# Kernel optimization log

Measured on AMD Instinct MI355X. Metric: run time of the kernel, lower is better.

## Reference

```python
import jax, jax.numpy as jnp
import numpy as np

EMBED_SIZE = 512
SCALE = EMBED_SIZE ** 0.5  # note: sqrt(embed_size), not sqrt(head_dim), per source


def setup_inputs() -> dict:
    key = jax.random.key(0)
    kq, kk, kv = jax.random.split(key, 3)
    B, H, S, D = 4, 8, 2048, 64
    query = jax.random.normal(kq, (B, H, S, D), dtype=jnp.float32)
    key_t = jax.random.normal(kk, (B, H, S, D), dtype=jnp.float32)
    value = jax.random.normal(kv, (B, S, H, D), dtype=jnp.float32)  # [b, kv_len, h, d]
    return {"query": query, "key": key_t, "value": value}


def reference(query, key, value):
    # scores: [b, h, q, k]
    scores = jnp.einsum('bhqf,bhkf->bhqk', query, key)
    weight = jax.nn.softmax(scores / SCALE, axis=3)
    # value is [b, l, h, d]; output [b, q, h, d]
    out = jnp.einsum('bhql,blhd->bqhd', weight, value)
    return out
```

## Files before the change

### kernel.cpp

```cpp
#include <hip/hip_runtime.h>
#include <stdint.h>

#define NB 4
#define NH 8
#define NS 2048
#define ND 64
#define BQ 128
#define TK 64
#define KP 72
#define NG 2
#define NITG (NS/(TK*NG))
#define SLOT (TK*KP + ND*KP)

typedef __bf16  bf16x8 __attribute__((ext_vector_type(8)));
typedef float   f32x16 __attribute__((ext_vector_type(16)));

__device__ __forceinline__ uint32_t pkbf(float x, float y) {
  uint32_t ax = __builtin_bit_cast(uint32_t, x) + 0x8000u;
  uint32_t ay = __builtin_bit_cast(uint32_t, y) + 0x8000u;
  return __builtin_amdgcn_perm(ay, ax, 0x07060302u);
}
__device__ __forceinline__ unsigned short bfu(float x) {
  return (unsigned short)((__builtin_bit_cast(uint32_t, x) + 0x8000u) >> 16);
}

__global__ __launch_bounds__(256) void prep(
    const float* __restrict__ K, const float* __restrict__ V,
    unsigned short* __restrict__ Kh, unsigned short* __restrict__ Vth)
{
  __shared__ unsigned short T[64*72];
  const int t = threadIdx.x;
  const int blk = blockIdx.x;
  const int bh = blk >> 5, st = blk & 31;
  const int s0 = st*64;
  const int b = bh>>3, hh = bh&7;

  {
    const float* kin = K + ((size_t)bh*NS + s0)*ND + t*16;
    unsigned short* kout = Kh + ((size_t)bh*NS + s0)*ND + t*16;
    float4 a0 = ((const float4*)kin)[0], a1 = ((const float4*)kin)[1];
    float4 a2 = ((const float4*)kin)[2], a3 = ((const float4*)kin)[3];
    uint4 w0 = make_uint4(pkbf(a0.x,a0.y),pkbf(a0.z,a0.w),pkbf(a1.x,a1.y),pkbf(a1.z,a1.w));
    uint4 w1 = make_uint4(pkbf(a2.x,a2.y),pkbf(a2.z,a2.w),pkbf(a3.x,a3.y),pkbf(a3.z,a3.w));
    ((uint4*)kout)[0] = w0; ((uint4*)kout)[1] = w1;
  }

  {
    const int vrow = t>>2, vq = t&3;
    const float* vp = V + (((size_t)b*NS + s0 + vrow)*NH + hh)*ND + 4*vq;
#pragma unroll
    for (int j=0;j<4;++j){
      float4 v = *(const float4*)(vp + 16*j);
      int d0 = 16*j + 4*vq;
      T[(size_t)(d0+0)*72 + vrow] = bfu(v.x);
      T[(size_t)(d0+1)*72 + vrow] = bfu(v.y);
      T[(size_t)(d0+2)*72 + vrow] = bfu(v.z);
      T[(size_t)(d0+3)*72 + vrow] = bfu(v.w);
    }
  }
  __syncthreads();
  {
    const int dd = t>>2, wq = t&3;
    unsigned short* vout = Vth + ((size_t)bh*ND + dd)*NS + s0 + 16*wq;
    uint4 o0 = *(const uint4*)&T[(size_t)dd*72 + 16*wq];
    uint4 o1 = *(const uint4*)&T[(size_t)dd*72 + 16*wq + 8];
    ((uint4*)vout)[0] = o0; ((uint4*)vout)[1] = o1;
  }
}

__global__ __launch_bounds__(512, 4) void fa_fwd(
    const float* __restrict__ Q, const unsigned short* __restrict__ Kh,
    const unsigned short* __restrict__ Vth, float* __restrict__ O)
{
  __shared__ __attribute__((aligned(16))) unsigned short SMEM[NG*2*SLOT];

  const int tid = threadIdx.x, wid = tid>>6, lane = tid&63;
  const int l31 = lane&31, h = lane>>5;
  const int g = wid>>2, qs = wid&3;
  const int t4 = tid & 255;

  const int bid = blockIdx.x;
  const int logical = (bid & 7)*64 + (bid >> 3);
  const int bh = logical >> 4;
  const int q0 = (logical & 15) * BQ;
  const int b = bh>>3, hh = bh&7;

  const float*          Qb  = Q   + ((size_t)bh*NS + q0)*ND;
  const unsigned short* Kb  = Kh  + (size_t)bh*NS*ND;
  const unsigned short* Vtb = Vth + (size_t)bh*ND*NS;
  float*                Ob  = O   + ((size_t)b*NS*NH + hh)*ND;

  const float kSc = 1.44269504088896340736f / 22.6274169979695207808f;

  bf16x8 qf[4];
  {
    const float* qp = Qb + (size_t)(qs*32 + l31)*ND + 8*h;
#pragma unroll
    for (int k=0;k<4;++k){
      float4 a = *(const float4*)(qp + 16*k);
      float4 c = *(const float4*)(qp + 16*k + 4);
      uint4 u = make_uint4(pkbf(a.x*kSc,a.y*kSc), pkbf(a.z*kSc,a.w*kSc),
                           pkbf(c.x*kSc,c.y*kSc), pkbf(c.z*kSc,c.w*kSc));
      qf[k] = __builtin_bit_cast(bf16x8, u);
    }
  }

  const int srow = t4>>3, soct = t4&7;

  uint4 stg[4];
  auto load_tile = [&](int kv0){
    const unsigned short* kp = Kb + (size_t)(kv0 + srow)*ND + 8*soct;
    stg[0] = *(const uint4*)kp;
    stg[1] = *(const uint4*)(kp + 32*ND);
    const unsigned short* vp = Vtb + (size_t)srow*NS + kv0 + 8*soct;
    stg[2] = *(const uint4*)vp;
    stg[3] = *(const uint4*)(vp + (size_t)32*NS);
  };
  auto store_tile = [&](int buf){
    unsigned short* Kl = SMEM + (size_t)(g*2+buf)*SLOT;
    unsigned short* Vt = Kl + TK*KP;
    *(uint4*)&Kl[(size_t)srow*KP + 8*soct] = stg[0];
    *(uint4*)&Kl[(size_t)(srow+32)*KP + 8*soct] = stg[1];
    *(uint4*)&Vt[(size_t)srow*KP + 8*soct] = stg[2];
    *(uint4*)&Vt[(size_t)(srow+32)*KP + 8*soct] = stg[3];
  };

  load_tile(g*NITG*TK);
  store_tile(0);
  __syncthreads();

  const f32x16 zero = {0,0,0,0,0,0,0,0,0,0,0,0,0,0,0,0};
  f32x16 acc[2] = {zero, zero};
  float lsum = 0.f;

  for (int t=0; t<NITG; ++t){
    const int cur = t&1;
    if (t+1 < NITG) load_tile((g*NITG + t + 1)*TK);

    const unsigned short* Kl = SMEM + (size_t)(g*2+cur)*SLOT;
    const unsigned short* Vt = Kl + TK*KP;

    f32x16 st[2];
    __builtin_amdgcn_s_setprio(1);
#pragma unroll
    for (int tt=0;tt<2;++tt){
      st[tt] = zero;
#pragma unroll
      for (int k=0;k<4;++k){
        bf16x8 kf = *(const bf16x8*)&Kl[(size_t)(32*tt+l31)*KP + 16*k + 8*h];
        st[tt] = __builtin_amdgcn_mfma_f32_32x32x16_bf16(kf, qf[k], st[tt], 0,0,0);
      }
    }
    __builtin_amdgcn_s_setprio(0);

    uint32_t P0[2][4], P1[2][4];
#pragma unroll
    for (int tt=0;tt<2;++tt)
#pragma unroll
      for (int u=0;u<4;++u){
        float p0 = __builtin_amdgcn_exp2f(st[tt][4*u+0]);
        float p1 = __builtin_amdgcn_exp2f(st[tt][4*u+1]);
        float p2 = __builtin_amdgcn_exp2f(st[tt][4*u+2]);
        float p3 = __builtin_amdgcn_exp2f(st[tt][4*u+3]);
        lsum += (p0+p1)+(p2+p3);
        P0[tt][u] = pkbf(p0,p1);
        P1[tt][u] = pkbf(p2,p3);
      }

    uint32_t X0[2][2], X1[2][2];
#pragma unroll
    for (int tt=0;tt<2;++tt)
#pragma unroll
      for (int m=0;m<2;++m){
        uint32_t y0 = h ? P0[tt][2*m] : P0[tt][2*m+1];
        uint32_t y1 = h ? P1[tt][2*m] : P1[tt][2*m+1];
        X0[tt][m] = (uint32_t)__shfl_xor((int)y0, 32, 64);
        X1[tt][m] = (uint32_t)__shfl_xor((int)y1, 32, 64);
      }
    bf16x8 pf[4];
#pragma unroll
    for (int k=0;k<4;++k){
      int tt = k>>1, m = k&1;
      uint32_t lo0 = h ? X0[tt][m]     : P0[tt][2*m];
      uint32_t lo1 = h ? X1[tt][m]     : P1[tt][2*m];
      uint32_t hi0 = h ? P0[tt][2*m+1] : X0[tt][m];
      uint32_t hi1 = h ? P1[tt][2*m+1] : X1[tt][m];
      uint4 u = make_uint4(lo0, lo1, hi0, hi1);
      pf[k] = __builtin_bit_cast(bf16x8, u);
    }

    __builtin_amdgcn_s_setprio(1);
#pragma unroll
    for (int gg=0;gg<2;++gg)
#pragma unroll
      for (int k=0;k<4;++k){
        bf16x8 vf = *(const bf16x8*)&Vt[(size_t)(32*gg+l31)*KP + 16*k + 8*h];
        acc[gg] = __builtin_amdgcn_mfma_f32_32x32x16_bf16(vf, pf[k], acc[gg], 0,0,0);
      }
    __builtin_amdgcn_s_setprio(0);

    if (t+1 < NITG) store_tile(cur^1);
    __syncthreads();
  }

  lsum += __shfl_xor(lsum, 32, 64);
  const int row = qs*32 + l31;
  float* accL = (float*)SMEM;
  float* lsL  = accL + 128*68;

  if (g==1){
#pragma unroll
    for (int gg=0; gg<2; ++gg)
#pragma unroll
      for (int u=0; u<4; ++u){
        float4 o;
        o.x = acc[gg][4*u+0]; o.y = acc[gg][4*u+1];
        o.z = acc[gg][4*u+2]; o.w = acc[gg][4*u+3];
        *(float4*)&accL[(size_t)row*68 + 32*gg + 8*u + 4*h] = o;
      }
    if (h==0) lsL[row] = lsum;
  }
  __syncthreads();
  if (g==0){
    const float inv = 1.0f/(lsum + lsL[row]);
    float* op = Ob + (size_t)(q0 + row)*(NH*ND);
#pragma unroll
    for (int gg=0; gg<2; ++gg)
#pragma unroll
      for (int u=0; u<4; ++u){
        float4 c = *(const float4*)&accL[(size_t)row*68 + 32*gg + 8*u + 4*h];
        float4 o;
        o.x = (acc[gg][4*u+0]+c.x)*inv;
        o.y = (acc[gg][4*u+1]+c.y)*inv;
        o.z = (acc[gg][4*u+2]+c.z)*inv;
        o.w = (acc[gg][4*u+3]+c.w)*inv;
        *(float4*)(op + 32*gg + 8*u + 4*h) = o;
      }
  }
}

extern "C" void kernel_launch(void* const* d_in, const int* in_sizes, int n_in,
                              void* d_out, int out_size, void* d_ws, size_t ws_size,
                              hipStream_t stream) {
  const float* Q = (const float*)d_in[0];
  const float* K = (const float*)d_in[1];
  const float* V = (const float*)d_in[2];
  float* O = (float*)d_out;
  unsigned short* Kh  = (unsigned short*)d_ws;
  unsigned short* Vth = Kh + (size_t)NB*NH*NS*ND;
  hipLaunchKernelGGL(prep, dim3(NB*NH*(NS/64)), dim3(256), 0, stream, K, V, Kh, Vth);
  dim3 grid((NS / BQ) * NB * NH);
  hipLaunchKernelGGL(fa_fwd, grid, dim3(512), 0, stream, Q, Kh, Vth, O);
}
```

Measured before the change: 158.2 us.

## Drop KV-split wave groups; use single 256-thread group with 128-key tiles

Removes the two-group split of the key/value range inside each block, so each block now runs 4 waves that walk the full sequence with 128-key tiles. The LDS-based cross-group reduction of accumulators and row sums at the end goes away. It also removes one block-wide barrier, and each tile barrier now synchronises fewer waves. The cost is fewer waves per block and larger tiles, with more staging registers and a different LDS footprint, which lowers latency hiding per block and changes occupancy.

```diff
diff --git a/kernel.cpp b/kernel.cpp
--- a/kernel.cpp
+++ b/kernel.cpp
@@ -6,11 +6,11 @@
 #define NS 2048
 #define ND 64
 #define BQ 128
-#define TK 64
+#define TK 128
 #define KP 72
-#define NG 2
-#define NITG (NS/(TK*NG))
-#define SLOT (TK*KP + ND*KP)
+#define VP 136
+#define NIT (NS/TK)
+#define SLOT (TK*KP + ND*VP)
 
 typedef __bf16  bf16x8 __attribute__((ext_vector_type(8)));
 typedef float   f32x16 __attribute__((ext_vector_type(16)));
@@ -68,16 +68,15 @@
   }
 }
 
-__global__ __launch_bounds__(512, 4) void fa_fwd(
+__global__ __launch_bounds__(256, 2) void fa_fwd(
     const float* __restrict__ Q, const unsigned short* __restrict__ Kh,
     const unsigned short* __restrict__ Vth, float* __restrict__ O)
 {
-  __shared__ __attribute__((aligned(16))) unsigned short SMEM[NG*2*SLOT];
+  __shared__ __attribute__((aligned(16))) unsigned short SMEM[2*SLOT];
 
   const int tid = threadIdx.x, wid = tid>>6, lane = tid&63;
   const int l31 = lane&31, h = lane>>5;
-  const int g = wid>>2, qs = wid&3;
-  const int t4 = tid & 255;
+  const int qs = wid;
 
   const int bid = blockIdx.x;
   const int logical = (bid & 7)*64 + (bid >> 3);
@@ -105,27 +104,35 @@
     }
   }
 
-  const int srow = t4>>3, soct = t4&7;
-
-  uint4 stg[4];
+  const int srow = tid>>3, soct = tid&7;
+
+  uint4 stg[8];
   auto load_tile = [&](int kv0){
-    const unsigned short* kp = Kb + (size_t)(kv0 + srow)*ND + 8*soct;
-    stg[0] = *(const uint4*)kp;
-    stg[1] = *(const uint4*)(kp + 32*ND);
-    const unsigned short* vp = Vtb + (size_t)srow*NS + kv0 + 8*soct;
-    stg[2] = *(const uint4*)vp;
-    stg[3] = *(const uint4*)(vp + (size_t)32*NS);
+#pragma unroll
+    for (int i=0;i<4;++i)
+      stg[i] = *(const uint4*)(Kb + (size_t)(kv0 + srow + 32*i)*ND + 8*soct);
+#pragma unroll
+    for (int j=0;j<2;++j){
+      const unsigned short* vp = Vtb + (size_t)(srow + 32*j)*NS + kv0 + 16*soct;
+      stg[4+2*j]   = ((const uint4*)vp)[0];
+      stg[4+2*j+1] = ((const uint4*)vp)[1];
+    }
   };
   auto store_tile = [&](int buf){
-    unsigned short* Kl = SMEM + (size_t)(g*2+buf)*SLOT;
+    unsigned short* Kl = SMEM + (size_t)buf*SLOT;
     unsigned short* Vt = Kl + TK*KP;
-    *(uint4*)&Kl[(size_t)srow*KP + 8*soct] = stg[0];
-    *(uint4*)&Kl[(size_t)(srow+32)*KP + 8*soct] = stg[1];
-    *(uint4*)&Vt[(size_t)srow*KP + 8*soct] = stg[2];
-    *(uint4*)&Vt[(size_t)(srow+32)*KP + 8*soct] = stg[3];
+#pragma unroll
+    for (int i=0;i<4;++i)
+      *(uint4*)&Kl[(size_t)(srow+32*i)*KP + 8*soct] = stg[i];
+#pragma unroll
+    for (int j=0;j<2;++j){
+      unsigned short* vq = &Vt[(size_t)(srow+32*j)*VP + 16*soct];
+      ((uint4*)vq)[0] = stg[4+2*j];
+      ((uint4*)vq)[1] = stg[4+2*j+1];
+    }
   };
 
-  load_tile(g*NITG*TK);
+  load_tile(0);
   store_tile(0);
   __syncthreads();
 
@@ -133,17 +140,17 @@
   f32x16 acc[2] = {zero, zero};
   float lsum = 0.f;
 
-  for (int t=0; t<NITG; ++t){
+  for (int t=0; t<NIT; ++t){
     const int cur = t&1;
-    if (t+1 < NITG) load_tile((g*NITG + t + 1)*TK);
-
-    const unsigned short* Kl = SMEM + (size_t)(g*2+cur)*SLOT;
+    if (t+1 < NIT) load_tile((t+1)*TK);
+
+    const unsigned short* Kl = SMEM + (size_t)cur*SLOT;
     const unsigned short* Vt = Kl + TK*KP;
 
-    f32x16 st[2];
+    f32x16 st[4];
     __builtin_amdgcn_s_setprio(1);
 #pragma unroll
-    for (int tt=0;tt<2;++tt){
+    for (int tt=0;tt<4;++tt){
       st[tt] = zero;
 #pragma unroll
       for (int k=0;k<4;++k){
@@ -153,9 +160,9 @@
     }
     __builtin_amdgcn_s_setprio(0);
 
-    uint32_t P0[2][4], P1[2][4];
-#pragma unroll
-    for (int tt=0;tt<2;++tt)
+    uint32_t P0[4][4], P1[4][4];
+#pragma unroll
+    for (int tt=0;tt<4;++tt)
 #pragma unroll
       for (int u=0;u<4;++u){
         float p0 = __builtin_amdgcn_exp2f(st[tt][4*u+0]);
@@ -167,9 +174,9 @@
         P1[tt][u] = pkbf(p2,p3);
       }
 
-    uint32_t X0[2][2], X1[2][2];
-#pragma unroll
-    for (int tt=0;tt<2;++tt)
+    uint32_t X0[4][2], X1[4][2];
+#pragma unroll
+    for (int tt=0;tt<4;++tt)
 #pragma unroll
       for (int m=0;m<2;++m){
         uint32_t y0 = h ? P0[tt][2*m] : P0[tt][2*m+1];
@@ -177,9 +184,9 @@
         X0[tt][m] = (uint32_t)__shfl_xor((int)y0, 32, 64);
         X1[tt][m] = (uint32_t)__shfl_xor((int)y1, 32, 64);
       }
-    bf16x8 pf[4];
-#pragma unroll
-    for (int k=0;k<4;++k){
+    bf16x8 pf[8];
+#pragma unroll
+    for (int k=0;k<8;++k){
       int tt = k>>1, m = k&1;
       uint32_t lo0 = h ? X0[tt][m]     : P0[tt][2*m];
       uint32_t lo1 = h ? X1[tt][m]     : P1[tt][2*m];
@@ -193,50 +200,31 @@
 #pragma unroll
     for (int gg=0;gg<2;++gg)
 #pragma unroll
-      for (int k=0;k<4;++k){
-        bf16x8 vf = *(const bf16x8*)&Vt[(size_t)(32*gg+l31)*KP + 16*k + 8*h];
+      for (int k=0;k<8;++k){
+        bf16x8 vf = *(const bf16x8*)&Vt[(size_t)(32*gg+l31)*VP + 16*k + 8*h];
         acc[gg] = __builtin_amdgcn_mfma_f32_32x32x16_bf16(vf, pf[k], acc[gg], 0,0,0);
       }
     __builtin_amdgcn_s_setprio(0);
 
-    if (t+1 < NITG) store_tile(cur^1);
+    if (t+1 < NIT) store_tile(cur^1);
     __syncthreads();
   }
 
   lsum += __shfl_xor(lsum, 32, 64);
-  const int row = qs*32 + l31;
-  float* accL = (float*)SMEM;
-  float* lsL  = accL + 128*68;
-
-  if (g==1){
-#pragma unroll
-    for (int gg=0; gg<2; ++gg)
-#pragma unroll
-      for (int u=0; u<4; ++u){
-        float4 o;
-        o.x = acc[gg][4*u+0]; o.y = acc[gg][4*u+1];
-        o.z = acc[gg][4*u+2]; o.w = acc[gg][4*u+3];
-        *(float4*)&accL[(size_t)row*68 + 32*gg + 8*u + 4*h] = o;
-      }
-    if (h==0) lsL[row] = lsum;
-  }
-  __syncthreads();
-  if (g==0){
-    const float inv = 1.0f/(lsum + lsL[row]);
-    float* op = Ob + (size_t)(q0 + row)*(NH*ND);
-#pragma unroll
-    for (int gg=0; gg<2; ++gg)
-#pragma unroll
-      for (int u=0; u<4; ++u){
-        float4 c = *(const float4*)&accL[(size_t)row*68 + 32*gg + 8*u + 4*h];
-        float4 o;
-        o.x = (acc[gg][4*u+0]+c.x)*inv;
-        o.y = (acc[gg][4*u+1]+c.y)*inv;
-        o.z = (acc[gg][4*u+2]+c.z)*inv;
-        o.w = (acc[gg][4*u+3]+c.w)*inv;
-        *(float4*)(op + 32*gg + 8*u + 4*h) = o;
-      }
-  }
+  const float inv = 1.0f / lsum;
+  const int q = q0 + qs*32 + l31;
+  float* op = Ob + (size_t)q*(NH*ND);
+#pragma unroll
+  for (int gg=0; gg<2; ++gg)
+#pragma unroll
+    for (int u=0; u<4; ++u){
+      float4 o;
+      o.x = acc[gg][4*u+0]*inv;
+      o.y = acc[gg][4*u+1]*inv;
+      o.z = acc[gg][4*u+2]*inv;
+      o.w = acc[gg][4*u+3]*inv;
+      *(float4*)(op + 32*gg + 8*u + 4*h) = o;
+    }
 }
 
 extern "C" void kernel_launch(void* const* d_in, const int* in_sizes, int n_in,
@@ -250,5 +238,5 @@
   unsigned short* Vth = Kh + (size_t)NB*NH*NS*ND;
   hipLaunchKernelGGL(prep, dim3(NB*NH*(NS/64)), dim3(256), 0, stream, K, V, Kh, Vth);
   dim3 grid((NS / BQ) * NB * NH);
-  hipLaunchKernelGGL(fa_fwd, grid, dim3(512), 0, stream, Q, Kh, Vth, O);
-}
+  hipLaunchKernelGGL(fa_fwd, grid, dim3(256), 0, stream, Q, Kh, Vth, O);
+}
```

Result: slower. 161.5 us (+2.1%).
